# Optimization experiments

Measured on AMD Instinct MI355X. Metric: run time of the kernel, lower is better.

The kernel has to match this reference:

```python
import jax, jax.numpy as jnp
import numpy as np

B, S, D_IN, D_OUT = 4, 2048, 4096, 4096


def setup_inputs() -> dict:
    key = jax.random.key(0)
    k1, k2, k3 = jax.random.split(key, 3)
    # int32 activations (already quantized upstream in the original pipeline)
    x_i32 = jax.random.randint(k1, (B, S, D_IN), -128, 128, dtype=jnp.int32)
    # int8 weights in [in, out] layout (Linear weight transposed), symmetric range [-127, 127]
    weight_i8 = jax.random.randint(k2, (D_IN, D_OUT), -127, 128, dtype=jnp.int32).astype(jnp.int8)
    # bias quantized affine to int32 (scale=16 in original)
    bias_i32 = jax.random.randint(k3, (D_OUT,), -2048, 2048, dtype=jnp.int32)
    return {"x_i32": x_i32, "weight_i8": weight_i8, "bias_i32": bias_i32, "out_shift": 7}


def reference(x_i32, weight_i8, bias_i32, out_shift):
    x_shape = x_i32.shape
    x2d = x_i32.reshape(-1, x_shape[-1]).astype(jnp.int32)  # [tokens, d_in]
    # int8 weights upcast to int32, plain int32 matmul with int32 accumulation
    y = jnp.matmul(x2d, weight_i8.astype(jnp.int32), preferred_element_type=jnp.int32)
    y = y + bias_i32  # fused bias add (int32)
    if out_shift > 0:  # out_shift is a static Python int
        y = jnp.right_shift(y, out_shift)  # arithmetic shift on signed int32
    return y.reshape(*x_shape[:-1], y.shape[-1]).astype(jnp.int32)
```

## Files before the change

kernel.cpp:

```cpp
#include <hip/hip_runtime.h>

using int32x4 = __attribute__((ext_vector_type(4))) int;

#define BM 256
#define BN 128
#define TBUF 24576

__global__ __launch_bounds__(256) void pack_x_kernel(const int32x4* __restrict__ x,
                                                     int32x4* __restrict__ xp,
                                                     int nvec) {
    int t = blockIdx.x * 256 + threadIdx.x;
    if (t >= nvec) return;
    int32x4 a = x[t * 4 + 0];
    int32x4 b = x[t * 4 + 1];
    int32x4 c = x[t * 4 + 2];
    int32x4 d = x[t * 4 + 3];
    int32x4 o;
    o.x = (a.x & 255) | ((a.y & 255) << 8) | ((a.z & 255) << 16) | (a.w << 24);
    o.y = (b.x & 255) | ((b.y & 255) << 8) | ((b.z & 255) << 16) | (b.w << 24);
    o.z = (c.x & 255) | ((c.y & 255) << 8) | ((c.z & 255) << 16) | (c.w << 24);
    o.w = (d.x & 255) | ((d.y & 255) << 8) | ((d.z & 255) << 16) | (d.w << 24);
    xp[t] = o;
}

__global__ __launch_bounds__(256) void transform_w_kernel(const int* __restrict__ w,
                                                          unsigned char* __restrict__ wt,
                                                          int K, int N) {
    __shared__ unsigned char tileT[64][72];
    int tx = threadIdx.x & 15;
    int ty = threadIdx.x >> 4;
    int n0 = blockIdx.x * 64;
    int k0 = blockIdx.y * 64;
#pragma unroll
    for (int r = 0; r < 4; ++r) {
        int row = ty * 4 + r;
        int32x4 v = *(const int32x4*)&w[(size_t)(k0 + row) * N + n0 + tx * 4];
        tileT[tx * 4 + 0][row] = (unsigned char)(v.x & 255);
        tileT[tx * 4 + 1][row] = (unsigned char)(v.y & 255);
        tileT[tx * 4 + 2][row] = (unsigned char)(v.z & 255);
        tileT[tx * 4 + 3][row] = (unsigned char)(v.w & 255);
    }
    __syncthreads();
#pragma unroll
    for (int r = 0; r < 4; ++r) {
        int row = ty * 4 + r;
        uchar4 v = *(const uchar4*)&tileT[row][tx * 4];
        *(uchar4*)&wt[(size_t)(n0 + row) * K + k0 + tx * 4] = v;
    }
}

__global__ __launch_bounds__(256, 2) void gemm_i8_3d(
    const char* __restrict__ A,
    const char* __restrict__ Bt,
    const int* __restrict__ bias,
    const int* __restrict__ shiftp,
    int* __restrict__ C,
    int M, int N, int K) {
    __shared__ char smem[3 * TBUF];

    const int nbn = N / BN;
    const int nwg = gridDim.x;
    const int bid = blockIdx.x;
    const int cpx = nwg >> 3;
    const int swz = (bid & 7) * cpx + (bid >> 3);
    const int m0 = (swz / nbn) * BM;
    const int n0 = (swz % nbn) * BN;

    const int t = threadIdx.x;
    const int lane = t & 63;
    const int wave = t >> 6;
    const int wr = wave >> 1;
    const int wc = wave & 1;

    const int s_row = t >> 2;
    const int s_col = ((t & 3) << 4) ^ (((t >> 3) & 3) << 4);
    const char* a_src = A + (size_t)(m0 + s_row) * K + s_col;
    const char* b_src = Bt + (size_t)(n0 + s_row) * K + s_col;
    const size_t jstr = (size_t)64 * K;
    char* lds_st = smem + t * 16;

    const int lr = lane & 15;
    const int lc = (lane >> 4) << 4;
    const int xr = ((lr >> 1) & 3) << 4;
    const int a_off = ((wr << 7) + lr) * 64 + (lc ^ xr);
    const int b_off = 16384 + ((wc << 6) + lr) * 64 + (lc ^ xr);

    int32x4 acc[8][4] = {};
    int32x4 af[4], ay[4], bf[4];

    const int nt = K / 64;

#define GLL(src, dst)                                                 \
    __builtin_amdgcn_global_load_lds(                                 \
        (const __attribute__((address_space(1))) void*)(src),        \
        (__attribute__((address_space(3))) void*)(dst), 16, 0, 0)

#define FENCE asm volatile("" ::: "memory")
#define BARR                           \
    do {                               \
        FENCE;                         \
        __builtin_amdgcn_s_barrier();  \
        FENCE;                         \
    } while (0)
#define SB0 __builtin_amdgcn_sched_barrier(0)
#define LGKM(n)                                                   \
    do {                                                          \
        asm volatile("s_waitcnt lgkmcnt(" #n ")" ::: "memory");   \
        SB0;                                                      \
    } while (0)
#define VMW(n)                                                  \
    do {                                                        \
        asm volatile("s_waitcnt vmcnt(" #n ")" ::: "memory");   \
        SB0;                                                    \
    } while (0)

#pragma unroll
    for (int p = 0; p < 2; ++p) {
#pragma unroll
        for (int j = 0; j < 4; ++j)
            GLL(a_src + (size_t)p * 64 + j * jstr, lds_st + p * TBUF + j * 4096);
#pragma unroll
        for (int j = 0; j < 2; ++j)
            GLL(b_src + (size_t)p * 64 + j * jstr, lds_st + p * TBUF + 16384 + j * 4096);
    }
    VMW(6);

    for (int tt = 0; tt < nt; ++tt) {
        const int base = (tt % 3) * TBUF;
        const int sb = ((tt + 2) % 3) * TBUF;
        const size_t kc = (size_t)(tt + 2) * 64;
        const bool st = (tt + 2) < nt;

        BARR;
#pragma unroll
        for (int i = 0; i < 4; ++i) af[i] = *(const int32x4*)&smem[base + a_off + i * 1024];
#pragma unroll
        for (int i = 0; i < 4; ++i) bf[i] = *(const int32x4*)&smem[base + b_off + i * 1024];
#pragma unroll
        for (int i = 0; i < 4; ++i) ay[i] = *(const int32x4*)&smem[base + a_off + (4 + i) * 1024];
        if (st) {
#pragma unroll
            for (int j = 0; j < 4; ++j)
                GLL(a_src + kc + j * jstr, lds_st + sb + j * 4096);
        }
        LGKM(4);
        __builtin_amdgcn_s_setprio(1);
#pragma unroll
        for (int mi = 0; mi < 4; ++mi)
#pragma unroll
            for (int ni = 0; ni < 4; ++ni)
                acc[mi][ni] = __builtin_amdgcn_mfma_i32_16x16x64_i8(af[mi], bf[ni], acc[mi][ni], 0, 0, 0);
        __builtin_amdgcn_s_setprio(0);
        if (st) {
#pragma unroll
            for (int j = 0; j < 2; ++j)
                GLL(b_src + kc + j * jstr, lds_st + sb + 16384 + j * 4096);
        }
        LGKM(0);
        __builtin_amdgcn_s_setprio(1);
#pragma unroll
        for (int mi = 0; mi < 4; ++mi)
#pragma unroll
            for (int ni = 0; ni < 4; ++ni)
                acc[4 + mi][ni] = __builtin_amdgcn_mfma_i32_16x16x64_i8(ay[mi], bf[ni], acc[4 + mi][ni], 0, 0, 0);
        __builtin_amdgcn_s_setprio(0);
        if (tt < nt - 2) {
            VMW(6);
        } else if (tt == nt - 2) {
            VMW(0);
        }
    }

    const int s = *shiftp;
    const int crow = (lane >> 4) << 2;
    const int ccol = lane & 15;
    int bv[4];
#pragma unroll
    for (int nf = 0; nf < 4; ++nf) bv[nf] = bias[n0 + wc * 64 + nf * 16 + ccol];
#pragma unroll
    for (int mf = 0; mf < 8; ++mf) {
        const int grow0 = m0 + wr * 128 + mf * 16 + crow;
#pragma unroll
        for (int nf = 0; nf < 4; ++nf) {
            const int gcol = n0 + wc * 64 + nf * 16 + ccol;
#pragma unroll
            for (int r = 0; r < 4; ++r) {
                int y = acc[mf][nf][r] + bv[nf];
                y = (s > 0) ? (y >> s) : y;
                C[(size_t)(grow0 + r) * N + gcol] = y;
            }
        }
    }
#undef GLL
#undef FENCE
#undef BARR
#undef SB0
#undef LGKM
#undef VMW
}

extern "C" void kernel_launch(void* const* d_in, const int* in_sizes, int n_in,
                              void* d_out, int out_size, void* d_ws, size_t ws_size,
                              hipStream_t stream) {
    const int* x = (const int*)d_in[0];
    const int* w = (const int*)d_in[1];
    const int* bias = (const int*)d_in[2];
    const int* shiftp = (const int*)d_in[3];
    int* out = (int*)d_out;

    const int N = in_sizes[2];
    const int K = in_sizes[1] / N;
    const int M = in_sizes[0] / K;

    char* xp = (char*)d_ws;
    unsigned char* wt = (unsigned char*)d_ws + (size_t)M * K;

    int nvec = (int)(((long long)M * K) / 16);
    pack_x_kernel<<<(nvec + 255) / 256, 256, 0, stream>>>((const int32x4*)x, (int32x4*)xp, nvec);

    dim3 tgrid(N / 64, K / 64);
    transform_w_kernel<<<tgrid, 256, 0, stream>>>(w, wt, K, N);

    int nwg = (M / BM) * (N / BN);
    gemm_i8_3d<<<nwg, 256, 0, stream>>>(xp, (const char*)wt, bias, shiftp, out, M, N, K);
}
```

Measured before the change: 197.1 us.

## Enlarge GEMM tile to 256x256 with 8 waves, K=128 steps, double buffering

The int8 GEMM moves from a 256x128 tile with 4 waves and a triple-buffered K=64 pipeline to a 256x256 tile with 8 waves (512 threads) and a double-buffered K=128 pipeline using 128 KB of LDS. Each wave now interleaves LDS fragment loads with four MFMA batches per stage. The larger tile raises arithmetic intensity and cuts global traffic per output. In exchange it uses far more LDS, which likely leaves one workgroup per CU despite the launch bound of 2. It also adds more barriers, and the stage loads are no longer overlapped with the previous buffer's compute as tightly.

```diff
diff --git a/kernel.cpp b/kernel.cpp
--- a/kernel.cpp
+++ b/kernel.cpp
@@ -3,8 +3,8 @@
 using int32x4 = __attribute__((ext_vector_type(4))) int;
 
 #define BM 256
-#define BN 128
-#define TBUF 24576
+#define BN 256
+#define MBUF 65536
 
 __global__ __launch_bounds__(256) void pack_x_kernel(const int32x4* __restrict__ x,
                                                      int32x4* __restrict__ xp,
@@ -49,14 +49,14 @@
     }
 }
 
-__global__ __launch_bounds__(256, 2) void gemm_i8_3d(
+__global__ __launch_bounds__(512, 2) void gemm_i8_mega(
     const char* __restrict__ A,
     const char* __restrict__ Bt,
     const int* __restrict__ bias,
     const int* __restrict__ shiftp,
     int* __restrict__ C,
     int M, int N, int K) {
-    __shared__ char smem[3 * TBUF];
+    __shared__ char smem[2 * MBUF];
 
     const int nbn = N / BN;
     const int nwg = gridDim.x;
@@ -69,11 +69,11 @@
     const int t = threadIdx.x;
     const int lane = t & 63;
     const int wave = t >> 6;
-    const int wr = wave >> 1;
-    const int wc = wave & 1;
-
-    const int s_row = t >> 2;
-    const int s_col = ((t & 3) << 4) ^ (((t >> 3) & 3) << 4);
+    const int wr = wave >> 2;
+    const int wc = wave & 3;
+
+    const int s_row = t >> 3;
+    const int s_col = (((t & 7) ^ ((t >> 3) & 7)) << 4);
     const char* a_src = A + (size_t)(m0 + s_row) * K + s_col;
     const char* b_src = Bt + (size_t)(n0 + s_row) * K + s_col;
     const size_t jstr = (size_t)64 * K;
@@ -81,14 +81,18 @@
 
     const int lr = lane & 15;
     const int lc = (lane >> 4) << 4;
-    const int xr = ((lr >> 1) & 3) << 4;
-    const int a_off = ((wr << 7) + lr) * 64 + (lc ^ xr);
-    const int b_off = 16384 + ((wc << 6) + lr) * 64 + (lc ^ xr);
+    const int xr = (lr & 7) << 4;
+    const int rowA = (wr << 7) + lr;
+    const int rowB = (wc << 6) + lr;
+    const int a_s0 = rowA * 128 + (lc ^ xr);
+    const int a_s1 = rowA * 128 + ((lc | 64) ^ xr);
+    const int b_s0 = 32768 + rowB * 128 + (lc ^ xr);
+    const int b_s1 = 32768 + rowB * 128 + ((lc | 64) ^ xr);
 
     int32x4 acc[8][4] = {};
-    int32x4 af[4], ay[4], bf[4];
-
-    const int nt = K / 64;
+    int32x4 afX[4], afY[4], bfX[4], bfY[4];
+
+    const int nt = K / 128;
 
 #define GLL(src, dst)                                                 \
     __builtin_amdgcn_global_load_lds(                                 \
@@ -114,62 +118,72 @@
         SB0;                                                    \
     } while (0)
 
-#pragma unroll
-    for (int p = 0; p < 2; ++p) {
-#pragma unroll
-        for (int j = 0; j < 4; ++j)
-            GLL(a_src + (size_t)p * 64 + j * jstr, lds_st + p * TBUF + j * 4096);
-#pragma unroll
-        for (int j = 0; j < 2; ++j)
-            GLL(b_src + (size_t)p * 64 + j * jstr, lds_st + p * TBUF + 16384 + j * 4096);
-    }
-    VMW(6);
-
-    for (int tt = 0; tt < nt; ++tt) {
-        const int base = (tt % 3) * TBUF;
-        const int sb = ((tt + 2) % 3) * TBUF;
-        const size_t kc = (size_t)(tt + 2) * 64;
-        const bool st = (tt + 2) < nt;
-
-        BARR;
-#pragma unroll
-        for (int i = 0; i < 4; ++i) af[i] = *(const int32x4*)&smem[base + a_off + i * 1024];
-#pragma unroll
-        for (int i = 0; i < 4; ++i) bf[i] = *(const int32x4*)&smem[base + b_off + i * 1024];
-#pragma unroll
-        for (int i = 0; i < 4; ++i) ay[i] = *(const int32x4*)&smem[base + a_off + (4 + i) * 1024];
-        if (st) {
-#pragma unroll
-            for (int j = 0; j < 4; ++j)
-                GLL(a_src + kc + j * jstr, lds_st + sb + j * 4096);
-        }
-        LGKM(4);
-        __builtin_amdgcn_s_setprio(1);
-#pragma unroll
-        for (int mi = 0; mi < 4; ++mi)
-#pragma unroll
-            for (int ni = 0; ni < 4; ++ni)
-                acc[mi][ni] = __builtin_amdgcn_mfma_i32_16x16x64_i8(af[mi], bf[ni], acc[mi][ni], 0, 0, 0);
-        __builtin_amdgcn_s_setprio(0);
-        if (st) {
-#pragma unroll
-            for (int j = 0; j < 2; ++j)
-                GLL(b_src + kc + j * jstr, lds_st + sb + 16384 + j * 4096);
-        }
-        LGKM(0);
-        __builtin_amdgcn_s_setprio(1);
-#pragma unroll
-        for (int mi = 0; mi < 4; ++mi)
-#pragma unroll
-            for (int ni = 0; ni < 4; ++ni)
-                acc[4 + mi][ni] = __builtin_amdgcn_mfma_i32_16x16x64_i8(ay[mi], bf[ni], acc[4 + mi][ni], 0, 0, 0);
-        __builtin_amdgcn_s_setprio(0);
-        if (tt < nt - 2) {
-            VMW(6);
-        } else if (tt == nt - 2) {
-            VMW(0);
-        }
-    }
+#define STAGE8(TT, BUF)                                                    \
+    do {                                                                   \
+        const size_t kc_ = (size_t)(TT) * 128;                             \
+        _Pragma("unroll") for (int j = 0; j < 4; ++j)                      \
+            GLL(a_src + kc_ + j * jstr, lds_st + (BUF) + j * 8192);        \
+        _Pragma("unroll") for (int j = 0; j < 4; ++j)                      \
+            GLL(b_src + kc_ + j * jstr, lds_st + (BUF) + 32768 + j * 8192);\
+    } while (0)
+
+#define MFMA_B(ACCROW, AF, BF)                                                   \
+    do {                                                                         \
+        __builtin_amdgcn_s_setprio(1);                                           \
+        _Pragma("unroll") for (int mi = 0; mi < 4; ++mi)                         \
+            _Pragma("unroll") for (int ni = 0; ni < 4; ++ni)                     \
+                acc[(ACCROW) + mi][ni] = __builtin_amdgcn_mfma_i32_16x16x64_i8(  \
+                    AF[mi], BF[ni], acc[(ACCROW) + mi][ni], 0, 0, 0);            \
+        __builtin_amdgcn_s_setprio(0);                                           \
+    } while (0)
+
+#define BODY(BUF)                                                                \
+    do {                                                                         \
+        _Pragma("unroll") for (int i = 0; i < 4; ++i)                            \
+            afX[i] = *(const int32x4*)&smem[(BUF) + a_s0 + i * 2048];            \
+        _Pragma("unroll") for (int i = 0; i < 4; ++i)                            \
+            bfX[i] = *(const int32x4*)&smem[(BUF) + b_s0 + i * 2048];            \
+        _Pragma("unroll") for (int i = 0; i < 4; ++i)                            \
+            afY[i] = *(const int32x4*)&smem[(BUF) + a_s0 + (4 + i) * 2048];      \
+        _Pragma("unroll") for (int i = 0; i < 4; ++i)                            \
+            bfY[i] = *(const int32x4*)&smem[(BUF) + b_s1 + i * 2048];            \
+        LGKM(8);                           \
+        MFMA_B(0, afX, bfX);                                                     \
+        LGKM(4);                                                  \
+        _Pragma("unroll") for (int i = 0; i < 4; ++i)                            \
+            afX[i] = *(const int32x4*)&smem[(BUF) + a_s1 + i * 2048];            \
+        MFMA_B(4, afY, bfX);                                                     \
+        LGKM(4);                               \
+        _Pragma("unroll") for (int i = 0; i < 4; ++i)                            \
+            afY[i] = *(const int32x4*)&smem[(BUF) + a_s1 + (4 + i) * 2048];      \
+        LGKM(4);                            \
+        MFMA_B(0, afX, bfY);                                                     \
+        LGKM(0);                                               \
+        MFMA_B(4, afY, bfY);                                                     \
+    } while (0)
+
+    STAGE8(0, 0);
+    STAGE8(1, MBUF);
+    VMW(8);
+    BARR;
+
+    for (int tt = 0; tt < nt - 2; tt += 2) {
+        BODY(0);
+        BARR;
+        STAGE8(tt + 2, 0);
+        VMW(8);
+        BARR;
+        BODY(MBUF);
+        BARR;
+        STAGE8(tt + 3, MBUF);
+        VMW(8);
+        BARR;
+    }
+    BODY(0);
+    BARR;
+    VMW(0);
+    BARR;
+    BODY(MBUF);
 
     const int s = *shiftp;
     const int crow = (lane >> 4) << 2;
@@ -197,6 +211,9 @@
 #undef SB0
 #undef LGKM
 #undef VMW
+#undef STAGE8
+#undef MFMA_B
+#undef BODY
 }
 
 extern "C" void kernel_launch(void* const* d_in, const int* in_sizes, int n_in,
@@ -222,5 +239,5 @@
     transform_w_kernel<<<tgrid, 256, 0, stream>>>(w, wt, K, N);
 
     int nwg = (M / BM) * (N / BN);
-    gemm_i8_3d<<<nwg, 256, 0, stream>>>(xp, (const char*)wt, bias, shiftp, out, M, N, K);
-}
+    gemm_i8_mega<<<nwg, 512, 0, stream>>>(xp, (const char*)wt, bias, shiftp, out, M, N, K);
+}
```

New measurement: 184.9 us. 6.2% less time.
